# Kernel optimization log

Hardware: AMD Instinct MI355X
Metric: run time of the kernel (lower is better)

## Reference

```python
import jax, jax.numpy as jnp
import numpy as np

DIM = 1024
HEADS = 16
HIDDEN = 2048  # dim * mlp_ratio
EPS = 1e-6


def _rmsnorm(x, scale):
    # faithful to torch: x * (scale / (norm / (sqrt(d) + eps)))
    norm = jnp.linalg.norm(x, axis=-1, keepdims=True)
    return x * (scale * (x.shape[-1] ** 0.5 + EPS) / norm)


def setup_inputs() -> dict:
    key = jax.random.key(0)
    ks = jax.random.split(key, 8)
    B, N, C = 4, 4096, DIM
    s = 0.02
    return {
        "x": jax.random.normal(ks[0], (B, N, C), dtype=jnp.float32),
        "scale1": jnp.ones((C,), jnp.float32),
        "scale2": jnp.ones((C,), jnp.float32),
        "gamma": jnp.ones((C,), jnp.float32),
        "qkv_w": jax.random.normal(ks[1], (3 * C, C), jnp.float32) * s,
        "proj_w": jax.random.normal(ks[2], (C, C), jnp.float32) * s,
        "proj_b": jnp.zeros((C,), jnp.float32),
        "conv1_w": jax.random.normal(ks[3], (HIDDEN, C), jnp.float32) * s,
        "conv1_b": jnp.zeros((HIDDEN,), jnp.float32),
        "conv2_w": jax.random.normal(ks[4], (C, HIDDEN), jnp.float32) * s,
        "conv2_b": jnp.zeros((C,), jnp.float32),
    }


def reference(x, scale1, scale2, gamma, qkv_w, proj_w, proj_b,
              conv1_w, conv1_b, conv2_w, conv2_b):
    B, N, C = x.shape
    h, d = HEADS, C // HEADS

    # ---- attention branch ----
    xn = _rmsnorm(x, scale1)
    qkv = jnp.einsum('bnc,fc->bnf', xn, qkv_w)           # [B,N,3C]
    qkv = qkv.reshape(B, N, 3, h, d).transpose(2, 0, 3, 1, 4)  # [3,B,h,N,d]
    q, k, v = qkv[0], qkv[1], qkv[2]
    phi = lambda t: jnp.exp(-0.5 * t * t)
    q, k = phi(q), phi(k)
    kv = jnp.einsum('bhnd,bhne->bhde', k, v)             # [B,h,d,d]
    z = 1.0 / (jnp.einsum('bhnd,bhd->bhn', q, k.sum(2)) + 1e-6)
    out = jnp.einsum('bhnd,bhde,bhn->bhne', q, kv, z)    # [B,h,N,d]
    out = out.transpose(0, 2, 1, 3).reshape(B, N, C)
    attn = jnp.einsum('bnc,oc->bno', out, proj_w) + proj_b
    x = x + gamma * attn

    # ---- MLP branch (1x1 convs == per-token linear) ----
    xn2 = _rmsnorm(x, scale2)
    hdd = jax.nn.gelu(jnp.einsum('bnc,hc->bnh', xn2, conv1_w) + conv1_b, approximate=False)
    mlp = jnp.einsum('bnh,ch->bnc', hdd, conv2_w) + conv2_b
    return x + gamma * mlp
```

## Files before the change

kernel.cpp:

```cpp
#include <hip/hip_runtime.h>
#include <hip/hip_bf16.h>
#include <math.h>

#define MTOK 16384

typedef __attribute__((ext_vector_type(8))) short bf16x8;
typedef __attribute__((ext_vector_type(4))) float f32x4;

__device__ __forceinline__ float bf2f(ushort u) {
  union { unsigned int u; float f; } c; c.u = ((unsigned int)u) << 16; return c.f;
}
__device__ __forceinline__ ushort f2bf(float f) {
  __hip_bfloat16 h = __float2bfloat16(f);
  return *(ushort*)&h;
}

__device__ __forceinline__ void gload_lds16(const void* g, void* l) {
  __builtin_amdgcn_global_load_lds(
      (const __attribute__((address_space(1))) unsigned int*)g,
      (__attribute__((address_space(3))) unsigned int*)l, 16, 0, 0);
}

__global__ __launch_bounds__(256)
void prep_k(const float* __restrict__ qkv_w, ushort* __restrict__ wq,
            const float* __restrict__ proj_w, ushort* __restrict__ wp,
            const float* __restrict__ conv1_w, ushort* __restrict__ w1,
            const float* __restrict__ conv2_w, ushort* __restrict__ w2,
            const float* __restrict__ gamma,
            const float* __restrict__ proj_b, const float* __restrict__ conv2_b,
            float* __restrict__ gbp, float* __restrict__ gbc,
            float* __restrict__ zero1, float* __restrict__ sumsq) {
  int b = blockIdx.x, t = threadIdx.x;
  if (b < 3072) {
    int i = b * 256 + t;
    float4 v = *(const float4*)&qkv_w[(size_t)i * 4];
    ushort4 o = {f2bf(v.x), f2bf(v.y), f2bf(v.z), f2bf(v.w)};
    *(ushort4*)&wq[(size_t)i * 4] = o;
  } else if (b < 4096) {
    int i = (b - 3072) * 256 + t;
    float g = gamma[(i * 4) >> 10];
    float4 v = *(const float4*)&proj_w[(size_t)i * 4];
    ushort4 o = {f2bf(v.x * g), f2bf(v.y * g), f2bf(v.z * g), f2bf(v.w * g)};
    *(ushort4*)&wp[(size_t)i * 4] = o;
  } else if (b < 6144) {
    int i = (b - 4096) * 256 + t;
    float4 v = *(const float4*)&conv1_w[(size_t)i * 4];
    ushort4 o = {f2bf(v.x), f2bf(v.y), f2bf(v.z), f2bf(v.w)};
    *(ushort4*)&w1[(size_t)i * 4] = o;
  } else if (b < 8192) {
    int i = (b - 6144) * 256 + t;
    float g = gamma[(i * 4) >> 11];
    float4 v = *(const float4*)&conv2_w[(size_t)i * 4];
    ushort4 o = {f2bf(v.x * g), f2bf(v.y * g), f2bf(v.z * g), f2bf(v.w * g)};
    *(ushort4*)&w2[(size_t)i * 4] = o;
  } else if (b < 8200) {
    int i = (b - 8192) * 256 + t;
    if (i < 1024) gbp[i] = gamma[i] * proj_b[i];
    else if (i < 2048) gbc[i - 1024] = gamma[i - 1024] * conv2_b[i - 1024];
  } else if (b < 8460) {
    int i = (b - 8200) * 256 + t;
    if (i < 66560) ((float4*)zero1)[i] = (float4){0.f, 0.f, 0.f, 0.f};
  } else {
    int i = (b - 8460) * 256 + t;
    if (i < 4096) ((float4*)sumsq)[i] = (float4){0.f, 0.f, 0.f, 0.f};
  }
}

__global__ __launch_bounds__(256)
void rn_k(const float* __restrict__ sumsq, float* __restrict__ rn, int n) {
  int i = blockIdx.x * 256 + threadIdx.x;
  if (i < n) rn[i] = (32.0f + 1e-6f) / sqrtf(sumsq[i]);
}

__global__ __launch_bounds__(256)
void rmsnorm_k(const float* __restrict__ x, const float* __restrict__ scale,
               ushort* __restrict__ out) {
  __shared__ float red[4];
  int row = blockIdx.x;
  int t = threadIdx.x;
  const float* xr = x + (size_t)row * 1024;
  float4 v = *(const float4*)&xr[t * 4];
  float s = v.x*v.x + v.y*v.y + v.z*v.z + v.w*v.w;
  #pragma unroll
  for (int off = 32; off > 0; off >>= 1) s += __shfl_xor(s, off);
  if ((t & 63) == 0) red[t >> 6] = s;
  __syncthreads();
  float tot = red[0] + red[1] + red[2] + red[3];
  float rn = (32.0f + 1e-6f) / sqrtf(tot);
  float4 sc = *(const float4*)&scale[t * 4];
  ushort4 o;
  o.x = f2bf(v.x * rn * sc.x);
  o.y = f2bf(v.y * rn * sc.y);
  o.z = f2bf(v.z * rn * sc.z);
  o.w = f2bf(v.w * rn * sc.w);
  *(ushort4*)&out[(size_t)row * 1024 + t * 4] = o;
}

template<int EPI>
__global__ __launch_bounds__(256, 2)
void gemm_bt(const ushort* __restrict__ A, const ushort* __restrict__ W,
             void* __restrict__ outp, const float* __restrict__ bias,
             const float* __restrict__ resid,
             ushort* __restrict__ kTp, ushort* __restrict__ vTp,
             const float* __restrict__ escale, const float* __restrict__ rowscale,
             float* __restrict__ sumsq, ushort* __restrict__ xnout,
             int M, int F, int K) {
  __shared__ ushort lA[2][128 * 32];
  __shared__ ushort lB[2][128 * 32];
  const int tid = threadIdx.x;
  const int lane = tid & 63;
  const int w = tid >> 6;
  const int nBn = F >> 7;
  const int cpx = (int)gridDim.x >> 3;
  const int tile = ((int)blockIdx.x & 7) * cpx + ((int)blockIdx.x >> 3);
  const int bm = tile / nBn;
  const int bn = tile % nBn;
  const int brow = bm << 7, bcol = bn << 7;
  const int wr = w >> 1, wc = w & 1;

  const int srow = (w << 4) + (lane >> 2);
  const int key = (srow >> 1) & 3;
  const int kcsrc = (lane & 3) ^ key;
  const ushort* gA0 = A + (size_t)(brow + srow) * K + kcsrc * 8;
  const ushort* gA1 = gA0 + (size_t)64 * K;
  const ushort* gB0 = W + (size_t)(bcol + srow) * K + kcsrc * 8;
  const ushort* gB1 = gB0 + (size_t)64 * K;

  auto stage = [&](int bf, int k0) {
    gload_lds16(gA0 + k0, &lA[bf][w * 512]);
    gload_lds16(gA1 + k0, &lA[bf][2048 + w * 512]);
    gload_lds16(gB0 + k0, &lB[bf][w * 512]);
    gload_lds16(gB1 + k0, &lB[bf][2048 + w * 512]);
  };

  const int frow = lane & 15;
  const int kq = lane >> 4;

  f32x4 acc[4][4];
  #pragma unroll
  for (int i = 0; i < 4; ++i)
    #pragma unroll
    for (int j = 0; j < 4; ++j) acc[i][j] = (f32x4){0.f, 0.f, 0.f, 0.f};

  stage(0, 0);
  __syncthreads();

  int buf = 0;
  for (int k0 = 0; k0 < K; k0 += 32, buf ^= 1) {
    if (k0 + 32 < K) stage(buf ^ 1, k0 + 32);

    bf16x8 af[4], bfr[4];
    #pragma unroll
    for (int mi = 0; mi < 4; ++mi) {
      int row = (wr << 6) + (mi << 4) + frow;
      int off = (row << 5) + ((kq ^ ((row >> 1) & 3)) << 3);
      af[mi] = *(const bf16x8*)&lA[buf][off];
    }
    #pragma unroll
    for (int ni = 0; ni < 4; ++ni) {
      int row = (wc << 6) + (ni << 4) + frow;
      int off = (row << 5) + ((kq ^ ((row >> 1) & 3)) << 3);
      bfr[ni] = *(const bf16x8*)&lB[buf][off];
    }
    #pragma unroll
    for (int mi = 0; mi < 4; ++mi)
      #pragma unroll
      for (int ni = 0; ni < 4; ++ni)
        acc[mi][ni] = __builtin_amdgcn_mfma_f32_16x16x32_bf16(
            af[mi], bfr[ni], acc[mi][ni], 0, 0, 0);
    __syncthreads();
  }

  #pragma unroll
  for (int mi = 0; mi < 4; ++mi) {
    const int rbase = brow + (wr << 6) + (mi << 4) + (kq << 2);
    float ss[4] = {0.f, 0.f, 0.f, 0.f};
    #pragma unroll
    for (int ni = 0; ni < 4; ++ni) {
      int col = bcol + (wc << 6) + (ni << 4) + frow;
      if (EPI == 0) {
        if (col < 1024) {
          #pragma unroll
          for (int r = 0; r < 4; ++r) {
            float v = acc[mi][ni][r];
            ((ushort*)outp)[(size_t)(rbase + r) * 1024 + col] =
                f2bf(__expf(-0.5f * v * v));
          }
        } else {
          bool isk = col < 2048;
          int c = col - (isk ? 1024 : 2048);
          int b = rbase >> 12, n = rbase & 4095;
          ushort4 o;
          #pragma unroll
          for (int r = 0; r < 4; ++r) {
            float v = acc[mi][ni][r];
            if (isk) v = __expf(-0.5f * v * v);
            ((ushort*)&o)[r] = f2bf(v);
          }
          ushort* dst = (isk ? kTp : vTp) +
                        ((size_t)(b * 16 + (c >> 6)) * 64 + (c & 63)) * 4096 + n;
          *(ushort4*)dst = o;
        }
      } else if (EPI == 1) {
        #pragma unroll
        for (int r = 0; r < 4; ++r) {
          size_t idx = (size_t)(rbase + r) * F + col;
          ((float*)outp)[idx] = resid[idx] + acc[mi][ni][r] + bias[col];
        }
      } else if (EPI == 2) {
        #pragma unroll
        for (int r = 0; r < 4; ++r) {
          float t2 = acc[mi][ni][r] * rowscale[rbase + r] + bias[col];
          float y = 0.79788456f * (t2 + 0.044715f * t2 * t2 * t2);
          float e = __expf(2.0f * y);
          float th = (e - 1.0f) / (e + 1.0f);
          ((ushort*)outp)[(size_t)(rbase + r) * F + col] =
              f2bf(0.5f * t2 * (1.0f + th));
        }
      } else {
        #pragma unroll
        for (int r = 0; r < 4; ++r) {
          size_t idx = (size_t)(rbase + r) * F + col;
          float x1 = resid[idx] + acc[mi][ni][r] + bias[col];
          ((float*)outp)[idx] = x1;
          xnout[idx] = f2bf(x1 * escale[col]);
          ss[r] += x1 * x1;
        }
      }
    }
    if (EPI == 3) {
      #pragma unroll
      for (int r = 0; r < 4; ++r) {
        #pragma unroll
        for (int m = 1; m < 16; m <<= 1) ss[r] += __shfl_xor(ss[r], m);
      }
      if (frow == 0) {
        #pragma unroll
        for (int r = 0; r < 4; ++r) atomicAdd(&sumsq[rbase + r], ss[r]);
      }
    }
  }
}

__global__ __launch_bounds__(256)
void attn_kv_mfma(const ushort* __restrict__ kT, const ushort* __restrict__ vT,
                  float* __restrict__ kvT, float* __restrict__ ksum) {
  __shared__ float red[4][4096];
  int bi = blockIdx.x;
  int ksl = bi & 7, h = (bi >> 3) & 15, b = bi >> 7;
  int tid = threadIdx.x, lane = tid & 63, w = tid >> 6;
  int frow = lane & 15, kq = lane >> 4;
  const size_t bh = (size_t)(b * 16 + h) * 64;
  const ushort* vb = vT + bh * 4096;
  const ushort* kb = kT + bh * 4096;
  int tk0 = ksl * 512 + w * 128;

  f32x4 acc[4][4];
  #pragma unroll
  for (int i = 0; i < 4; ++i)
    #pragma unroll
    for (int j = 0; j < 4; ++j) acc[i][j] = (f32x4){0.f, 0.f, 0.f, 0.f};
  float kpart[4] = {0.f, 0.f, 0.f, 0.f};

  #pragma unroll
  for (int kstep = 0; kstep < 4; ++kstep) {
    int tok = tk0 + kstep * 32 + kq * 8;
    bf16x8 af[4], bfr[4];
    #pragma unroll
    for (int mi = 0; mi < 4; ++mi)
      af[mi] = *(const bf16x8*)&vb[(size_t)(mi * 16 + frow) * 4096 + tok];
    #pragma unroll
    for (int ni = 0; ni < 4; ++ni) {
      bfr[ni] = *(const bf16x8*)&kb[(size_t)(ni * 16 + frow) * 4096 + tok];
      #pragma unroll
      for (int j = 0; j < 8; ++j) kpart[ni] += bf2f((ushort)bfr[ni][j]);
    }
    #pragma unroll
    for (int mi = 0; mi < 4; ++mi)
      #pragma unroll
      for (int ni = 0; ni < 4; ++ni)
        acc[mi][ni] = __builtin_amdgcn_mfma_f32_16x16x32_bf16(
            af[mi], bfr[ni], acc[mi][ni], 0, 0, 0);
  }

  #pragma unroll
  for (int ni = 0; ni < 4; ++ni) {
    kpart[ni] += __shfl_xor(kpart[ni], 16);
    kpart[ni] += __shfl_xor(kpart[ni], 32);
  }
  if (lane < 16) {
    #pragma unroll
    for (int ni = 0; ni < 4; ++ni)
      atomicAdd(&ksum[(b * 16 + h) * 64 + ni * 16 + frow], kpart[ni]);
  }

  #pragma unroll
  for (int mi = 0; mi < 4; ++mi)
    #pragma unroll
    for (int ni = 0; ni < 4; ++ni)
      #pragma unroll
      for (int r = 0; r < 4; ++r)
        red[w][(mi * 16 + kq * 4 + r) * 64 + ni * 16 + frow] = acc[mi][ni][r];
  __syncthreads();
  float* kvg = kvT + (size_t)(b * 16 + h) * 4096;
  for (int i = tid; i < 4096; i += 256) {
    float s = red[0][i] + red[1][i] + red[2][i] + red[3][i];
    atomicAdd(&kvg[i], s);
  }
}

__global__ __launch_bounds__(256)
void attn_out_mfma(const ushort* __restrict__ qb, const float* __restrict__ kvT,
                   const float* __restrict__ ksum, ushort* __restrict__ ao) {
  __shared__ ushort skv[64 * 72];
  __shared__ float sks[64];
  int bi = blockIdx.x;
  int c = bi & 15, h = (bi >> 4) & 15, b = bi >> 8;
  int tid = threadIdx.x, lane = tid & 63, w = tid >> 6;
  int frow = lane & 15, kq = lane >> 4;
  const float* kvg = kvT + (size_t)(b * 16 + h) * 4096;
  for (int i = tid; i < 4096; i += 256)
    skv[(i >> 6) * 72 + (i & 63)] = f2bf(kvg[i]);
  if (tid < 64) sks[tid] = ksum[(b * 16 + h) * 64 + tid];
  __syncthreads();

  int m0 = b * 4096 + c * 256 + w * 64;
  f32x4 acc[4][4];
  #pragma unroll
  for (int i = 0; i < 4; ++i)
    #pragma unroll
    for (int j = 0; j < 4; ++j) acc[i][j] = (f32x4){0.f, 0.f, 0.f, 0.f};
  float dp[4] = {0.f, 0.f, 0.f, 0.f};

  #pragma unroll
  for (int kst = 0; kst < 2; ++kst) {
    int d0 = kst * 32 + kq * 8;
    bf16x8 af[4], bfr[4];
    #pragma unroll
    for (int mi = 0; mi < 4; ++mi)
      af[mi] = *(const bf16x8*)&qb[(size_t)(m0 + mi * 16 + frow) * 1024 + h * 64 + d0];
    #pragma unroll
    for (int ni = 0; ni < 4; ++ni)
      bfr[ni] = *(const bf16x8*)&skv[(ni * 16 + frow) * 72 + d0];
    #pragma unroll
    for (int mi = 0; mi < 4; ++mi) {
      float s = 0.f;
      #pragma unroll
      for (int j = 0; j < 8; ++j) s += bf2f((ushort)af[mi][j]) * sks[d0 + j];
      dp[mi] += s;
    }
    #pragma unroll
    for (int mi = 0; mi < 4; ++mi)
      #pragma unroll
      for (int ni = 0; ni < 4; ++ni)
        acc[mi][ni] = __builtin_amdgcn_mfma_f32_16x16x32_bf16(
            af[mi], bfr[ni], acc[mi][ni], 0, 0, 0);
  }

  #pragma unroll
  for (int mi = 0; mi < 4; ++mi) {
    dp[mi] += __shfl_xor(dp[mi], 16);
    dp[mi] += __shfl_xor(dp[mi], 32);
  }

  #pragma unroll
  for (int mi = 0; mi < 4; ++mi)
    #pragma unroll
    for (int ni = 0; ni < 4; ++ni)
      #pragma unroll
      for (int r = 0; r < 4; ++r) {
        float dotv = __shfl(dp[mi], (kq << 2) + r);
        float z = 1.f / (dotv + 1e-6f);
        int mrow = m0 + mi * 16 + kq * 4 + r;
        ao[(size_t)mrow * 1024 + h * 64 + ni * 16 + frow] =
            f2bf(acc[mi][ni][r] * z);
      }
}

extern "C" void kernel_launch(void* const* d_in, const int* in_sizes, int n_in,
                              void* d_out, int out_size, void* d_ws, size_t ws_size,
                              hipStream_t stream) {
  const float* x       = (const float*)d_in[0];
  const float* scale1  = (const float*)d_in[1];
  const float* scale2  = (const float*)d_in[2];
  const float* gamma   = (const float*)d_in[3];
  const float* qkv_w   = (const float*)d_in[4];
  const float* proj_w  = (const float*)d_in[5];
  const float* proj_b  = (const float*)d_in[6];
  const float* conv1_w = (const float*)d_in[7];
  const float* conv1_b = (const float*)d_in[8];
  const float* conv2_w = (const float*)d_in[9];
  const float* conv2_b = (const float*)d_in[10];
  float* out = (float*)d_out;

  char* ws = (char*)d_ws;
  size_t off = 0;
  auto alloc = [&](size_t bytes) {
    void* p = ws + off;
    off += (bytes + 255) & ~(size_t)255;
    return p;
  };
  ushort* xn     = (ushort*)alloc((size_t)MTOK * 1024 * 2);
  ushort* qb     = (ushort*)alloc((size_t)MTOK * 1024 * 2);
  ushort* kT     = (ushort*)alloc((size_t)MTOK * 1024 * 2);
  ushort* vT     = (ushort*)alloc((size_t)MTOK * 1024 * 2);
  ushort* attn_o = (ushort*)alloc((size_t)MTOK * 1024 * 2);
  float*  kvT    = (float*)alloc((size_t)(4 * 16 * 64 * 64 + 4 * 16 * 64) * 4);
  float*  ksum   = kvT + 4 * 16 * 64 * 64;
  ushort* wq = (ushort*)alloc((size_t)3072 * 1024 * 2);
  ushort* wp = (ushort*)alloc((size_t)1024 * 1024 * 2);
  ushort* w1 = (ushort*)alloc((size_t)2048 * 1024 * 2);
  ushort* w2 = (ushort*)alloc((size_t)1024 * 2048 * 2);
  float*  gbp = (float*)alloc(1024 * 4);
  float*  gbc = (float*)alloc(1024 * 4);
  float*  sumsq = (float*)alloc(MTOK * 4);
  float*  rnb   = (float*)alloc(MTOK * 4);
  ushort* hid = kT;
  if (off > ws_size) return;

  prep_k<<<8476, 256, 0, stream>>>(qkv_w, wq, proj_w, wp, conv1_w, w1, conv2_w, w2,
                                   gamma, proj_b, conv2_b, gbp, gbc, kvT, sumsq);

  rmsnorm_k<<<MTOK, 256, 0, stream>>>(x, scale1, xn);
  gemm_bt<0><<<128 * 24, 256, 0, stream>>>(xn, wq, qb, nullptr, nullptr,
                                           kT, vT, nullptr, nullptr, nullptr, nullptr,
                                           MTOK, 3072, 1024);
  attn_kv_mfma<<<512, 256, 0, stream>>>(kT, vT, kvT, ksum);
  attn_out_mfma<<<1024, 256, 0, stream>>>(qb, kvT, ksum, attn_o);
  gemm_bt<3><<<128 * 8, 256, 0, stream>>>(attn_o, wp, out, gbp, x,
                                          nullptr, nullptr, scale2, nullptr,
                                          sumsq, xn, MTOK, 1024, 1024);
  rn_k<<<64, 256, 0, stream>>>(sumsq, rnb, MTOK);

  gemm_bt<2><<<128 * 16, 256, 0, stream>>>(xn, w1, hid, conv1_b, nullptr,
                                           nullptr, nullptr, nullptr, rnb,
                                           nullptr, nullptr, MTOK, 2048, 1024);
  gemm_bt<1><<<128 * 8, 256, 0, stream>>>(hid, w2, out, gbc, out,
                                          nullptr, nullptr, nullptr, nullptr,
                                          nullptr, nullptr, MTOK, 1024, 2048);
}
```

Baseline: 448.5 us.

## Use 8-wave GEMM blocks and fold rmsnorm and rn kernels elsewhere

Each 128x128 GEMM block now runs 8 waves instead of 4, with each wave owning a 64x32 sub-tile, so each thread issues half as many loads and accumulates half as many tiles. The aim is to raise wave-level parallelism and hide latency. The first rmsnorm is merged into the prep kernel as extra blocks, and rn_k is removed: the GELU GEMM epilogue computes the row scale directly from sumsq with an rsqrt. The costs are more LDS fragment reads per block, since A fragments are now shared by four waves, and tighter register limits from the new launch bounds. The unseen EPI==3 row-sum reduction must also still match the new wave mapping.

```diff
diff --git a/kernel.cpp b/kernel.cpp
--- a/kernel.cpp
+++ b/kernel.cpp
@@ -29,7 +29,9 @@
             const float* __restrict__ gamma,
             const float* __restrict__ proj_b, const float* __restrict__ conv2_b,
             float* __restrict__ gbp, float* __restrict__ gbc,
-            float* __restrict__ zero1, float* __restrict__ sumsq) {
+            float* __restrict__ zero1, float* __restrict__ sumsq,
+            const float* __restrict__ x, const float* __restrict__ scale1,
+            ushort* __restrict__ xn) {
   int b = blockIdx.x, t = threadIdx.x;
   if (b < 3072) {
     int i = b * 256 + t;
@@ -60,49 +62,38 @@
   } else if (b < 8460) {
     int i = (b - 8200) * 256 + t;
     if (i < 66560) ((float4*)zero1)[i] = (float4){0.f, 0.f, 0.f, 0.f};
-  } else {
+  } else if (b < 8476) {
     int i = (b - 8460) * 256 + t;
     if (i < 4096) ((float4*)sumsq)[i] = (float4){0.f, 0.f, 0.f, 0.f};
-  }
-}
-
-__global__ __launch_bounds__(256)
-void rn_k(const float* __restrict__ sumsq, float* __restrict__ rn, int n) {
-  int i = blockIdx.x * 256 + threadIdx.x;
-  if (i < n) rn[i] = (32.0f + 1e-6f) / sqrtf(sumsq[i]);
-}
-
-__global__ __launch_bounds__(256)
-void rmsnorm_k(const float* __restrict__ x, const float* __restrict__ scale,
-               ushort* __restrict__ out) {
-  __shared__ float red[4];
-  int row = blockIdx.x;
-  int t = threadIdx.x;
-  const float* xr = x + (size_t)row * 1024;
-  float4 v = *(const float4*)&xr[t * 4];
-  float s = v.x*v.x + v.y*v.y + v.z*v.z + v.w*v.w;
-  #pragma unroll
-  for (int off = 32; off > 0; off >>= 1) s += __shfl_xor(s, off);
-  if ((t & 63) == 0) red[t >> 6] = s;
-  __syncthreads();
-  float tot = red[0] + red[1] + red[2] + red[3];
-  float rn = (32.0f + 1e-6f) / sqrtf(tot);
-  float4 sc = *(const float4*)&scale[t * 4];
-  ushort4 o;
-  o.x = f2bf(v.x * rn * sc.x);
-  o.y = f2bf(v.y * rn * sc.y);
-  o.z = f2bf(v.z * rn * sc.z);
-  o.w = f2bf(v.w * rn * sc.w);
-  *(ushort4*)&out[(size_t)row * 1024 + t * 4] = o;
+  } else {
+    __shared__ float red[4];
+    int row = b - 8476;
+    const float* xr = x + (size_t)row * 1024;
+    float4 v = *(const float4*)&xr[t * 4];
+    float s = v.x*v.x + v.y*v.y + v.z*v.z + v.w*v.w;
+    #pragma unroll
+    for (int off = 32; off > 0; off >>= 1) s += __shfl_xor(s, off);
+    if ((t & 63) == 0) red[t >> 6] = s;
+    __syncthreads();
+    float tot = red[0] + red[1] + red[2] + red[3];
+    float rn = (32.0f + 1e-6f) / sqrtf(tot);
+    float4 sc = *(const float4*)&scale1[t * 4];
+    ushort4 o;
+    o.x = f2bf(v.x * rn * sc.x);
+    o.y = f2bf(v.y * rn * sc.y);
+    o.z = f2bf(v.z * rn * sc.z);
+    o.w = f2bf(v.w * rn * sc.w);
+    *(ushort4*)&xn[(size_t)row * 1024 + t * 4] = o;
+  }
 }
 
 template<int EPI>
-__global__ __launch_bounds__(256, 2)
+__global__ __launch_bounds__(512, 6)
 void gemm_bt(const ushort* __restrict__ A, const ushort* __restrict__ W,
              void* __restrict__ outp, const float* __restrict__ bias,
              const float* __restrict__ resid,
              ushort* __restrict__ kTp, ushort* __restrict__ vTp,
-             const float* __restrict__ escale, const float* __restrict__ rowscale,
+             const float* __restrict__ escale, const float* __restrict__ sumsq_in,
              float* __restrict__ sumsq, ushort* __restrict__ xnout,
              int M, int F, int K) {
   __shared__ ushort lA[2][128 * 32];
@@ -110,37 +101,33 @@
   const int tid = threadIdx.x;
   const int lane = tid & 63;
   const int w = tid >> 6;
+  const int wm = w >> 2, wn = w & 3;
   const int nBn = F >> 7;
   const int cpx = (int)gridDim.x >> 3;
   const int tile = ((int)blockIdx.x & 7) * cpx + ((int)blockIdx.x >> 3);
   const int bm = tile / nBn;
   const int bn = tile % nBn;
   const int brow = bm << 7, bcol = bn << 7;
-  const int wr = w >> 1, wc = w & 1;
 
   const int srow = (w << 4) + (lane >> 2);
   const int key = (srow >> 1) & 3;
   const int kcsrc = (lane & 3) ^ key;
   const ushort* gA0 = A + (size_t)(brow + srow) * K + kcsrc * 8;
-  const ushort* gA1 = gA0 + (size_t)64 * K;
   const ushort* gB0 = W + (size_t)(bcol + srow) * K + kcsrc * 8;
-  const ushort* gB1 = gB0 + (size_t)64 * K;
 
   auto stage = [&](int bf, int k0) {
     gload_lds16(gA0 + k0, &lA[bf][w * 512]);
-    gload_lds16(gA1 + k0, &lA[bf][2048 + w * 512]);
     gload_lds16(gB0 + k0, &lB[bf][w * 512]);
-    gload_lds16(gB1 + k0, &lB[bf][2048 + w * 512]);
   };
 
   const int frow = lane & 15;
   const int kq = lane >> 4;
 
-  f32x4 acc[4][4];
+  f32x4 acc[4][2];
   #pragma unroll
   for (int i = 0; i < 4; ++i)
     #pragma unroll
-    for (int j = 0; j < 4; ++j) acc[i][j] = (f32x4){0.f, 0.f, 0.f, 0.f};
+    for (int j = 0; j < 2; ++j) acc[i][j] = (f32x4){0.f, 0.f, 0.f, 0.f};
 
   stage(0, 0);
   __syncthreads();
@@ -149,23 +136,23 @@
   for (int k0 = 0; k0 < K; k0 += 32, buf ^= 1) {
     if (k0 + 32 < K) stage(buf ^ 1, k0 + 32);
 
-    bf16x8 af[4], bfr[4];
+    bf16x8 af[4], bfr[2];
     #pragma unroll
     for (int mi = 0; mi < 4; ++mi) {
-      int row = (wr << 6) + (mi << 4) + frow;
+      int row = (wm << 6) + (mi << 4) + frow;
       int off = (row << 5) + ((kq ^ ((row >> 1) & 3)) << 3);
       af[mi] = *(const bf16x8*)&lA[buf][off];
     }
     #pragma unroll
-    for (int ni = 0; ni < 4; ++ni) {
-      int row = (wc << 6) + (ni << 4) + frow;
+    for (int ni = 0; ni < 2; ++ni) {
+      int row = (wn << 5) + (ni << 4) + frow;
       int off = (row << 5) + ((kq ^ ((row >> 1) & 3)) << 3);
       bfr[ni] = *(const bf16x8*)&lB[buf][off];
     }
     #pragma unroll
     for (int mi = 0; mi < 4; ++mi)
       #pragma unroll
-      for (int ni = 0; ni < 4; ++ni)
+      for (int ni = 0; ni < 2; ++ni)
         acc[mi][ni] = __builtin_amdgcn_mfma_f32_16x16x32_bf16(
             af[mi], bfr[ni], acc[mi][ni], 0, 0, 0);
     __syncthreads();
@@ -173,11 +160,17 @@
 
   #pragma unroll
   for (int mi = 0; mi < 4; ++mi) {
-    const int rbase = brow + (wr << 6) + (mi << 4) + (kq << 2);
+    const int rbase = brow + (wm << 6) + (mi << 4) + (kq << 2);
     float ss[4] = {0.f, 0.f, 0.f, 0.f};
-    #pragma unroll
-    for (int ni = 0; ni < 4; ++ni) {
-      int col = bcol + (wc << 6) + (ni << 4) + frow;
+    float rsc[4];
+    if (EPI == 2) {
+      #pragma unroll
+      for (int r = 0; r < 4; ++r)
+        rsc[r] = (32.0f + 1e-6f) * __frsqrt_rn(sumsq_in[rbase + r]);
+    }
+    #pragma unroll
+    for (int ni = 0; ni < 2; ++ni) {
+      int col = bcol + (wn << 5) + (ni << 4) + frow;
       if (EPI == 0) {
         if (col < 1024) {
           #pragma unroll
@@ -210,7 +203,7 @@
       } else if (EPI == 2) {
         #pragma unroll
         for (int r = 0; r < 4; ++r) {
-          float t2 = acc[mi][ni][r] * rowscale[rbase + r] + bias[col];
+          float t2 = acc[mi][ni][r] * rsc[r] + bias[col];
           float y = 0.79788456f * (t2 + 0.044715f * t2 * t2 * t2);
           float e = __expf(2.0f * y);
           float th = (e - 1.0f) / (e + 1.0f);
@@ -414,28 +407,26 @@
   float*  gbp = (float*)alloc(1024 * 4);
   float*  gbc = (float*)alloc(1024 * 4);
   float*  sumsq = (float*)alloc(MTOK * 4);
-  float*  rnb   = (float*)alloc(MTOK * 4);
   ushort* hid = kT;
   if (off > ws_size) return;
 
-  prep_k<<<8476, 256, 0, stream>>>(qkv_w, wq, proj_w, wp, conv1_w, w1, conv2_w, w2,
-                                   gamma, proj_b, conv2_b, gbp, gbc, kvT, sumsq);
-
-  rmsnorm_k<<<MTOK, 256, 0, stream>>>(x, scale1, xn);
-  gemm_bt<0><<<128 * 24, 256, 0, stream>>>(xn, wq, qb, nullptr, nullptr,
+  prep_k<<<8476 + MTOK, 256, 0, stream>>>(qkv_w, wq, proj_w, wp, conv1_w, w1,
+                                          conv2_w, w2, gamma, proj_b, conv2_b,
+                                          gbp, gbc, kvT, sumsq, x, scale1, xn);
+
+  gemm_bt<0><<<128 * 24, 512, 0, stream>>>(xn, wq, qb, nullptr, nullptr,
                                            kT, vT, nullptr, nullptr, nullptr, nullptr,
                                            MTOK, 3072, 1024);
   attn_kv_mfma<<<512, 256, 0, stream>>>(kT, vT, kvT, ksum);
   attn_out_mfma<<<1024, 256, 0, stream>>>(qb, kvT, ksum, attn_o);
-  gemm_bt<3><<<128 * 8, 256, 0, stream>>>(attn_o, wp, out, gbp, x,
+  gemm_bt<3><<<128 * 8, 512, 0, stream>>>(attn_o, wp, out, gbp, x,
                                           nullptr, nullptr, scale2, nullptr,
                                           sumsq, xn, MTOK, 1024, 1024);
-  rn_k<<<64, 256, 0, stream>>>(sumsq, rnb, MTOK);
-
-  gemm_bt<2><<<128 * 16, 256, 0, stream>>>(xn, w1, hid, conv1_b, nullptr,
-                                           nullptr, nullptr, nullptr, rnb,
+
+  gemm_bt<2><<<128 * 16, 512, 0, stream>>>(xn, w1, hid, conv1_b, nullptr,
+                                           nullptr, nullptr, nullptr, sumsq,
                                            nullptr, nullptr, MTOK, 2048, 1024);
-  gemm_bt<1><<<128 * 8, 256, 0, stream>>>(hid, w2, out, gbc, out,
+  gemm_bt<1><<<128 * 8, 512, 0, stream>>>(hid, w2, out, gbc, out,
                                           nullptr, nullptr, nullptr, nullptr,
                                           nullptr, nullptr, MTOK, 1024, 2048);
 }
```

New measurement: 470.9 us. 5.0% more time.
